# Optimization experiments

Measured on AMD Instinct MI355X. Metric: run time of the kernel, lower is better.

Reference implementation:

```python
import jax, jax.numpy as jnp
import numpy as np

B, N, D = 16, 8192, 256
H = D // 2
N_PARCELS = 64          # number of parcel labels in the stage lookup
K_PER_PARCEL = 32       # allocation m for every parcel (self.values)
TAU = 1.0               # gumbel-softmax temperature


def setup_inputs() -> dict:
    key = jax.random.key(0)
    ks = jax.random.split(key, 6)
    patches = jax.random.normal(ks[0], (B, N, D), dtype=jnp.float32)
    features = jax.random.normal(ks[1], (B, N, D), dtype=jnp.float32)
    W1 = jax.random.normal(ks[2], (D, H), dtype=jnp.float32) * 0.05
    b1 = jnp.zeros((H,), dtype=jnp.float32)
    W2 = jax.random.normal(ks[3], (H,), dtype=jnp.float32) * 0.05  # fc2 weight, out_dim=1 squeezed
    b2 = jnp.zeros((), dtype=jnp.float32)
    # pre-sampled Gumbel(0,1) noise (torch F.gumbel_softmax samples internally)
    gumbel = jax.random.gumbel(ks[4], (B, N), dtype=jnp.float32)
    # flat per-patch parcel label, identical across batch (lookup.reshape(-1)[:N])
    lookup = (jnp.arange(N, dtype=jnp.int32) % N_PARCELS)
    return {"patches": patches, "features": features, "W1": W1, "b1": b1,
            "W2": W2, "b2": b2, "gumbel": gumbel, "lookup": lookup}


def reference(patches, features, W1, b1, W2, b2, gumbel, lookup):
    # tiny MLP: fc1 -> relu -> fc2 -> squeeze(-1)
    hidden = jax.nn.relu(jnp.einsum('bnd,dh->bnh', features, W1) + b1)
    importance_logits = jnp.einsum('bnh,h->bn', hidden, W2) + b2          # [B, N]
    # soft gumbel-softmax scores over the patch axis
    scores = jax.nn.softmax((importance_logits + gumbel) / TAU, axis=-1)  # [B, N]

    labels = jnp.arange(N_PARCELS, dtype=lookup.dtype)

    def per_parcel(label):
        m = lookup == label                                # [N], same for all batches
        masked = jnp.where(m[None, :], scores, -jnp.inf)   # [B, N]
        _, idx = jax.lax.top_k(masked, K_PER_PARCEL)       # [B, K]
        return idx

    idx_pbk = jax.vmap(per_parcel)(labels)                 # [P, B, K]
    all_selected_indices = jnp.transpose(idx_pbk, (1, 0, 2)).reshape(B, N_PARCELS * K_PER_PARCEL)

    # scatter 1.0 at selected positions
    final_mask = jnp.zeros_like(scores).at[jnp.arange(B)[:, None], all_selected_indices].set(1.0)
    # straight-through: value == final_mask, grad flows as -d(logits)
    mask_grad = final_mask + jax.lax.stop_gradient(importance_logits) - importance_logits

    final_patches = patches * mask_grad[..., None]                         # [B, N, D]
    selected_patches = jnp.take_along_axis(final_patches, all_selected_indices[..., None], axis=1)
    return selected_patches, all_selected_indices, importance_logits
```

## Files before the change

### kernel.cpp

```cpp
#include <hip/hip_runtime.h>
#include <hip/hip_bf16.h>

#define NB 16
#define NN 8192
#define ND 256
#define NH 128
#define NPARCEL 64
#define KSEL 32

typedef __attribute__((ext_vector_type(8))) short short8;
typedef __attribute__((ext_vector_type(4))) float floatx4;
typedef __attribute__((ext_vector_type(4))) float f32x4;

__device__ __forceinline__ unsigned short f2b(float x) {
    unsigned u = __builtin_bit_cast(unsigned, x);
    u += 0x7fffu + ((u >> 16) & 1u);
    return (unsigned short)(u >> 16);
}
__device__ __forceinline__ float b2f(unsigned short h) {
    return __builtin_bit_cast(float, (unsigned)h << 16);
}


__global__ __launch_bounds__(256) void k_prep(const float* __restrict__ W1,
                                              unsigned short* __restrict__ W1S) {
    int i = blockIdx.x * 256 + threadIdx.x;
    int k = i >> 7;
    int h = i & 127;
    float w = W1[i];
    unsigned short hi = f2b(w);
    unsigned short lo = f2b(w - b2f(hi));
    int p   = k >> 6;
    int kk6 = k & 63;
    int swz = (h & 7) << 4;
    unsigned char* base = (unsigned char*)W1S + p * 32768;
    int linh = h * 128 + kk6 * 2;
    int linl = 16384 + linh;
    *(unsigned short*)(base + (linh ^ swz)) = hi;
    *(unsigned short*)(base + (linl ^ swz)) = lo;
}

__global__ __launch_bounds__(256, 4) void k_mlp(const float* __restrict__ feat,
                                                const unsigned short* __restrict__ W1S,
                                                const float* __restrict__ b1,
                                                const float* __restrict__ W2,
                                                const float* __restrict__ b2,
                                                float* __restrict__ out_logit) {
    __shared__ f32x4 lds4[2048];
    unsigned char* lds = (unsigned char*)lds4;

    const int tid  = threadIdx.x;
    const int wave = tid >> 6;
    const int lane = tid & 63;
    const int quad = lane >> 4;
    const int m    = lane & 15;
    const int wavebase = blockIdx.x * 128 + wave * 32;

    const float* ap0 = feat + (size_t)(wavebase + m) * ND + quad * 8;
    const float* ap1 = ap0 + 16 * ND;
    const int swz = (m & 7) << 4;

    floatx4 acc[2][8];
#pragma unroll
    for (int rg = 0; rg < 2; ++rg)
#pragma unroll
        for (int nt = 0; nt < 8; ++nt) acc[rg][nt] = (floatx4){0.f, 0.f, 0.f, 0.f};

#pragma unroll 1
    for (int p = 0; p < 4; ++p) {
        if (p) __syncthreads();
        const f32x4* src = (const f32x4*)((const unsigned char*)W1S + p * 32768);
#pragma unroll
        for (int i = 0; i < 8; ++i) lds4[tid + i * 256] = src[tid + i * 256];
        __syncthreads();

#pragma unroll 1
        for (int kx = 0; kx < 2; ++kx) {
            const int k0 = p * 64 + kx * 32;
            f32x4 a00 = *(const f32x4*)(ap0 + k0);
            f32x4 a01 = *(const f32x4*)(ap0 + k0 + 4);
            f32x4 a10 = *(const f32x4*)(ap1 + k0);
            f32x4 a11 = *(const f32x4*)(ap1 + k0 + 4);

            short8 ah0, al0, ah1, al1;
#pragma unroll
            for (int j = 0; j < 8; ++j) {
                float x0 = (j < 4) ? a00[j] : a01[j - 4];
                unsigned short h0 = f2b(x0);
                ah0[j] = (short)h0;
                al0[j] = (short)f2b(x0 - b2f(h0));
                float x1 = (j < 4) ? a10[j] : a11[j - 4];
                unsigned short h1 = f2b(x1);
                ah1[j] = (short)h1;
                al1[j] = (short)f2b(x1 - b2f(h1));
            }

            const int rb = (m * 128 + quad * 16 + kx * 64) ^ swz;
#pragma unroll
            for (int nt = 0; nt < 8; ++nt) {
                short8 bh = *(const short8*)(lds + (rb + nt * 2048));
                short8 bl = *(const short8*)(lds + (rb + nt * 2048 + 16384));
                acc[0][nt] = __builtin_amdgcn_mfma_f32_16x16x32_bf16(ah0, bh, acc[0][nt], 0, 0, 0);
                acc[0][nt] = __builtin_amdgcn_mfma_f32_16x16x32_bf16(ah0, bl, acc[0][nt], 0, 0, 0);
                acc[0][nt] = __builtin_amdgcn_mfma_f32_16x16x32_bf16(al0, bh, acc[0][nt], 0, 0, 0);
                acc[1][nt] = __builtin_amdgcn_mfma_f32_16x16x32_bf16(ah1, bh, acc[1][nt], 0, 0, 0);
                acc[1][nt] = __builtin_amdgcn_mfma_f32_16x16x32_bf16(ah1, bl, acc[1][nt], 0, 0, 0);
                acc[1][nt] = __builtin_amdgcn_mfma_f32_16x16x32_bf16(al1, bh, acc[1][nt], 0, 0, 0);
            }
        }
    }

    const float b2v = b2[0];
#pragma unroll
    for (int rg = 0; rg < 2; ++rg) {
        float s[4] = {0.f, 0.f, 0.f, 0.f};
#pragma unroll
        for (int nt = 0; nt < 8; ++nt) {
            float b1f = b1[nt * 16 + m];
            float w2f = W2[nt * 16 + m];
#pragma unroll
            for (int r = 0; r < 4; ++r) {
                float h = acc[rg][nt][r] + b1f;
                s[r] += (h > 0.f ? h : 0.f) * w2f;
            }
        }
#pragma unroll
        for (int off = 1; off < 16; off <<= 1) {
#pragma unroll
            for (int r = 0; r < 4; ++r) s[r] += __shfl_xor(s[r], off, 64);
        }
        if (m == 0) {
            int rowbase = wavebase + rg * 16 + quad * 4;
#pragma unroll
            for (int r = 0; r < 4; ++r) {
                int row = rowbase + r;
                out_logit[row] = s[r] + b2v;
            }
        }
    }
}

__global__ __launch_bounds__(256) void k_topk_gather(const float* __restrict__ logit,
                                                     const float* __restrict__ gum,
                                                     const float* __restrict__ patches,
                                                     float* __restrict__ out_sel,
                                                     float* __restrict__ out_idx) {
    const int b = blockIdx.x >> 6;
    const int p = blockIdx.x & 63;
    const int t = threadIdx.x;
    const int g = t >> 6;
    const int l = t & 63;

    const float* lb = logit + b * NN;
    const float* gb = gum + b * NN;
    int i0 = p + 64 * l;
    int i1 = i0 + 4096;
    float v0 = lb[i0] + gb[i0];
    float v1 = lb[i1] + gb[i1];
    const int obase = b * (NPARCEL * KSEL) + p * KSEL;

    int idxs[8];
#pragma unroll
    for (int r = 0; r < KSEL; ++r) {
        float bv; int bi;
        if (v0 > v1 || (v0 == v1 && i0 < i1)) { bv = v0; bi = i0; }
        else                                  { bv = v1; bi = i1; }
#pragma unroll
        for (int off = 1; off < 64; off <<= 1) {
            float ov = __shfl_xor(bv, off, 64);
            int   oi = __shfl_xor(bi, off, 64);
            if (ov > bv || (ov == bv && oi < bi)) { bv = ov; bi = oi; }
        }
        if      (bi == i0) { v0 = -__builtin_inff(); i0 = 0x7fffffff; }
        else if (bi == i1) { v1 = -__builtin_inff(); i1 = 0x7fffffff; }
        int safe = bi & (NN - 1);
        if (t == r) out_idx[obase + r] = (float)safe;
        if ((r & 3) == g) idxs[r >> 2] = safe;
    }

#pragma unroll
    for (int rr = 0; rr < 8; ++rr) {
        const int r = rr * 4 + g;
        f32x4 v = *((const f32x4*)(patches + ((size_t)b * NN + idxs[rr]) * ND) + l);
        *((f32x4*)(out_sel + (size_t)(obase + r) * ND) + l) = v;
    }
}

extern "C" void kernel_launch(void* const* d_in, const int* in_sizes, int n_in,
                              void* d_out, int out_size, void* d_ws, size_t ws_size,
                              hipStream_t stream) {
    const float* patches = (const float*)d_in[0];
    const float* feat    = (const float*)d_in[1];
    const float* W1      = (const float*)d_in[2];
    const float* b1      = (const float*)d_in[3];
    const float* W2      = (const float*)d_in[4];
    const float* b2      = (const float*)d_in[5];
    const float* gum     = (const float*)d_in[6];

    float* out       = (float*)d_out;
    float* out_sel   = out;
    float* out_idx   = out + 8388608;
    float* out_logit = out + 8388608 + 32768;

    unsigned short* W1S = (unsigned short*)(out_sel);

    k_prep<<<128, 256, 0, stream>>>(W1, W1S);
    k_mlp<<<(NB * NN) / 128, 256, 0, stream>>>(feat, W1S, b1, W2, b2, out_logit);
    k_topk_gather<<<NB * NPARCEL, 256, 0, stream>>>(out_logit, gum, patches, out_sel, out_idx);
}
```

Baseline: 305.8 us.

## Double-buffer W1 slices in LDS and prefetch feature tiles in k_mlp

The MLP kernel now prefetches the next 64-wide K slice of the split-bf16 W1 and the next feature rows into registers while MFMAs run on the current slice. LDS holds two W1 slices, so the global loads of slice p+1 overlap compute on slice p instead of stalling behind a barrier. LDS doubles to 64KB per block and register use grows, so the launch bound drops from 4 to 2 blocks per CU, which may reduce latency hiding.

```diff
diff --git a/kernel.cpp b/kernel.cpp
--- a/kernel.cpp
+++ b/kernel.cpp
@@ -40,13 +40,13 @@
     *(unsigned short*)(base + (linl ^ swz)) = lo;
 }
 
-__global__ __launch_bounds__(256, 4) void k_mlp(const float* __restrict__ feat,
+__global__ __launch_bounds__(256, 2) void k_mlp(const float* __restrict__ feat,
                                                 const unsigned short* __restrict__ W1S,
                                                 const float* __restrict__ b1,
                                                 const float* __restrict__ W2,
                                                 const float* __restrict__ b2,
                                                 float* __restrict__ out_logit) {
-    __shared__ f32x4 lds4[2048];
+    __shared__ f32x4 lds4[4096];
     unsigned char* lds = (unsigned char*)lds4;
 
     const int tid  = threadIdx.x;
@@ -59,37 +59,58 @@
     const float* ap0 = feat + (size_t)(wavebase + m) * ND + quad * 8;
     const float* ap1 = ap0 + 16 * ND;
     const int swz = (m & 7) << 4;
+    const f32x4* w1 = (const f32x4*)W1S;
 
     floatx4 acc[2][8];
 #pragma unroll
     for (int rg = 0; rg < 2; ++rg)
 #pragma unroll
         for (int nt = 0; nt < 8; ++nt) acc[rg][nt] = (floatx4){0.f, 0.f, 0.f, 0.f};
+
+    f32x4 stg[8];
+#pragma unroll
+    for (int i = 0; i < 8; ++i) stg[i] = w1[tid + i * 256];
+    f32x4 avc[8];
+    avc[0] = *(const f32x4*)(ap0);
+    avc[1] = *(const f32x4*)(ap0 + 4);
+    avc[2] = *(const f32x4*)(ap1);
+    avc[3] = *(const f32x4*)(ap1 + 4);
+    avc[4] = *(const f32x4*)(ap0 + 32);
+    avc[5] = *(const f32x4*)(ap0 + 36);
+    avc[6] = *(const f32x4*)(ap1 + 32);
+    avc[7] = *(const f32x4*)(ap1 + 36);
+#pragma unroll
+    for (int i = 0; i < 8; ++i) lds4[tid + i * 256] = stg[i];
 
 #pragma unroll 1
     for (int p = 0; p < 4; ++p) {
-        if (p) __syncthreads();
-        const f32x4* src = (const f32x4*)((const unsigned char*)W1S + p * 32768);
-#pragma unroll
-        for (int i = 0; i < 8; ++i) lds4[tid + i * 256] = src[tid + i * 256];
         __syncthreads();
-
-#pragma unroll 1
+        f32x4 avn[8];
+        if (p < 3) {
+#pragma unroll
+            for (int i = 0; i < 8; ++i) stg[i] = w1[(p + 1) * 2048 + tid + i * 256];
+            const int kn = (p + 1) * 64;
+            avn[0] = *(const f32x4*)(ap0 + kn);
+            avn[1] = *(const f32x4*)(ap0 + kn + 4);
+            avn[2] = *(const f32x4*)(ap1 + kn);
+            avn[3] = *(const f32x4*)(ap1 + kn + 4);
+            avn[4] = *(const f32x4*)(ap0 + kn + 32);
+            avn[5] = *(const f32x4*)(ap0 + kn + 36);
+            avn[6] = *(const f32x4*)(ap1 + kn + 32);
+            avn[7] = *(const f32x4*)(ap1 + kn + 36);
+        }
+
+        unsigned char* cb = lds + (p & 1) * 32768;
+#pragma unroll
         for (int kx = 0; kx < 2; ++kx) {
-            const int k0 = p * 64 + kx * 32;
-            f32x4 a00 = *(const f32x4*)(ap0 + k0);
-            f32x4 a01 = *(const f32x4*)(ap0 + k0 + 4);
-            f32x4 a10 = *(const f32x4*)(ap1 + k0);
-            f32x4 a11 = *(const f32x4*)(ap1 + k0 + 4);
-
             short8 ah0, al0, ah1, al1;
 #pragma unroll
             for (int j = 0; j < 8; ++j) {
-                float x0 = (j < 4) ? a00[j] : a01[j - 4];
+                float x0 = (j < 4) ? avc[kx * 4 + 0][j] : avc[kx * 4 + 1][j - 4];
                 unsigned short h0 = f2b(x0);
                 ah0[j] = (short)h0;
                 al0[j] = (short)f2b(x0 - b2f(h0));
-                float x1 = (j < 4) ? a10[j] : a11[j - 4];
+                float x1 = (j < 4) ? avc[kx * 4 + 2][j] : avc[kx * 4 + 3][j - 4];
                 unsigned short h1 = f2b(x1);
                 ah1[j] = (short)h1;
                 al1[j] = (short)f2b(x1 - b2f(h1));
@@ -98,8 +119,8 @@
             const int rb = (m * 128 + quad * 16 + kx * 64) ^ swz;
 #pragma unroll
             for (int nt = 0; nt < 8; ++nt) {
-                short8 bh = *(const short8*)(lds + (rb + nt * 2048));
-                short8 bl = *(const short8*)(lds + (rb + nt * 2048 + 16384));
+                short8 bh = *(const short8*)(cb + (rb + nt * 2048));
+                short8 bl = *(const short8*)(cb + (rb + nt * 2048 + 16384));
                 acc[0][nt] = __builtin_amdgcn_mfma_f32_16x16x32_bf16(ah0, bh, acc[0][nt], 0, 0, 0);
                 acc[0][nt] = __builtin_amdgcn_mfma_f32_16x16x32_bf16(ah0, bl, acc[0][nt], 0, 0, 0);
                 acc[0][nt] = __builtin_amdgcn_mfma_f32_16x16x32_bf16(al0, bh, acc[0][nt], 0, 0, 0);
@@ -107,6 +128,14 @@
                 acc[1][nt] = __builtin_amdgcn_mfma_f32_16x16x32_bf16(ah1, bl, acc[1][nt], 0, 0, 0);
                 acc[1][nt] = __builtin_amdgcn_mfma_f32_16x16x32_bf16(al1, bh, acc[1][nt], 0, 0, 0);
             }
+        }
+        __syncthreads();
+        if (p < 3) {
+            const int nb = ((p + 1) & 1) * 2048;
+#pragma unroll
+            for (int i = 0; i < 8; ++i) lds4[nb + tid + i * 256] = stg[i];
+#pragma unroll
+            for (int i = 0; i < 8; ++i) avc[i] = avn[i];
         }
     }
 
```

Measured after the change: 306.2 us. Within noise of the previous version (+0.1%).
